# Kernel tuning notes

Measured on AMD Instinct MI355X. Metric: run time of the kernel, lower is better.

The kernel has to match this reference:

```python
import jax, jax.numpy as jnp
import numpy as np
from jax import lax

UNITS = 128
NUM_STEPS = 2048
BATCH = 32
MIN_OMEGA = 0.1
MAX_OMEGA = 70.1
DT = 1.0 / 173.61          # EEG sampling interval
INPUT_SCALER = 0.1
BETA = 0.01
TWO_PI = 2 * 3.1415        # module uses 3.1415, not math.pi


def setup_inputs() -> dict:
    key = jax.random.key(0)
    k1, k2 = jax.random.split(key)
    X_r = jax.random.normal(k1, (BATCH, NUM_STEPS, UNITS), dtype=jnp.float32)
    X_i = jax.random.normal(k2, (BATCH, NUM_STEPS, UNITS), dtype=jnp.float32)
    omegas = (jnp.linspace(MIN_OMEGA, MAX_OMEGA, UNITS) * TWO_PI).astype(jnp.float32)[None, :]  # [1, U]
    return {"X_r": X_r, "X_i": X_i, "omegas": omegas}


def reference(X_r, X_i, omegas):
    B, T, U = X_r.shape
    r0 = jnp.ones((B, U), dtype=X_r.dtype)
    phi0 = jnp.zeros((B, U), dtype=X_r.dtype)

    def step(carry, xs):
        r, phi = carry
        xr, xi = xs  # [B, U] each
        input_r = INPUT_SCALER * xr * jnp.cos(phi)
        input_phi = INPUT_SCALER * xi * jnp.sin(phi)
        r = r + ((1.0 - BETA * jnp.square(r)) * r + input_r) * DT
        phi = phi + (omegas - input_phi) * DT
        return (r, phi), (r, phi)

    xs = (jnp.transpose(X_r, (1, 0, 2)), jnp.transpose(X_i, (1, 0, 2)))  # [T, B, U]
    _, (r_seq, phi_seq) = lax.scan(step, (r0, phi0), xs)
    r = jnp.transpose(r_seq, (1, 0, 2))    # [B, T, U]
    phi = jnp.transpose(phi_seq, (1, 0, 2))
    z_real = r * jnp.cos(phi)
    z_imag = r * jnp.sin(phi)
    return (z_real, z_imag)
```

## Files before the change

### kernel.cpp

```cpp
#include <hip/hip_runtime.h>
#include <math.h>

namespace {
constexpr int kUnits = 128;
constexpr int kSteps = 2048;
constexpr int kBatch = 32;
constexpr int kSeg = 16;
constexpr int kNSeg = kSteps / kSeg;
constexpr int kUBlk = 16;
constexpr int kUPT = 2;
constexpr int kUG = kUBlk / kUPT;
constexpr int kThreads = kUG * kNSeg;
constexpr int kBlocks = kBatch * (kUnits / kUBlk);
constexpr int kGrp = 16;
constexpr int kGrpSeg = kNSeg / kGrp;
constexpr int kPad = kUBlk + 1;
constexpr double kDT = 1.0 / 173.61;
constexpr double kTwoPi = 6.283185307179586;
constexpr double kInv2Pi = 1.0 / kTwoPi;
constexpr size_t kChainElems = (size_t)kSteps * kUnits;

typedef float v2f __attribute__((ext_vector_type(2)));

struct Tables {
  float G[kSteps];
  float Gseg[kNSeg];
  float Gg[kGrp];
  float rbar0[kNSeg];
};
constexpr Tables make_tables() {
  Tables tb{};
  double r = 1.0;
  for (int t = 0; t < kSteps; ++t) {
    if (t % kSeg == 0) tb.rbar0[t / kSeg] = (float)r;
    tb.G[t] = (float)(1.0 + (1.0 - 0.03 * r * r) * kDT);
    r = r + (1.0 - 0.01 * r * r) * r * kDT;
  }
  for (int s = 0; s < kNSeg; ++s) {
    double p = 1.0;
    for (int j = 0; j < kSeg; ++j) p *= (double)tb.G[s * kSeg + j];
    tb.Gseg[s] = (float)p;
  }
  for (int g = 0; g < kGrp; ++g) {
    double p = 1.0;
    for (int s = 0; s < kGrpSeg; ++s) p *= (double)tb.Gseg[g * kGrpSeg + s];
    tb.Gg[g] = (float)p;
  }
  return tb;
}
}

__constant__ Tables kTab = make_tables();

__global__ __launch_bounds__(kThreads)
void hopf_fused(const float* __restrict__ Xr, const float* __restrict__ Xi,
                const float* __restrict__ Om,
                float* __restrict__ Zr, float* __restrict__ Zi) {
  __shared__ float sG[kNSeg][kPad];
  __shared__ float sH[kNSeg][kPad];
  __shared__ float sP[kNSeg][kPad];
  __shared__ float sQ[kNSeg][kPad];
  __shared__ float cG[kGrp][kPad], cH[kGrp][kPad], cP[kGrp][kPad], cQ[kGrp][kPad];
  __shared__ float pD[kGrp][kPad], pR[kGrp][kPad];

  const int tid = threadIdx.x;
  const int ug = tid & (kUG - 1);
  const int seg = tid >> 3;
  const int b = blockIdx.x >> 3;
  const int uq = blockIdx.x & 7;
  const int u0 = uq * kUBlk + ug * kUPT;
  const int t0 = seg * kSeg;

  float cw[kUPT], sw[kUPT], c0[kUPT], s0[kUPT];
  double wdt_d[kUPT];
#pragma unroll
  for (int k = 0; k < kUPT; ++k) {
    const double wdt = (double)Om[u0 + k] * kDT;
    wdt_d[k] = wdt;
    double sd, cd;
    sincos(wdt, &sd, &cd);
    cw[k] = (float)cd;
    sw[k] = (float)sd;
    const double ang = wdt * (double)t0;
    const double kk = rint(ang * kInv2Pi);
    const float th = (float)fma(-kk, kTwoPi, ang);
    __sincosf(th, &s0[k], &c0[k]);
  }

  const size_t base = ((size_t)b * kSteps + t0) * (size_t)kUnits + u0;
  const v2f* xr2 = (const v2f*)(Xr + base);
  const v2f* xi2 = (const v2f*)(Xi + base);
  v2f xr[kSeg], xi[kSeg];
#pragma unroll
  for (int j = 0; j < kSeg; ++j) {
    xr[j] = xr2[j * (kUnits / 2)];
    xi[j] = xi2[j * (kUnits / 2)];
  }

  const float cdt = (float)(0.1 * kDT);
  float gr[kUPT] = {1.f, 1.f}, hr[kUPT] = {0.f, 0.f};
  float pr[kUPT] = {0.f, 0.f}, qr[kUPT] = {0.f, 0.f};
#pragma unroll
  for (int j = 0; j < kSeg; ++j) {
    const float Ge = kTab.G[t0 + j];
#pragma unroll
    for (int k = 0; k < kUPT; ++k) {
      const float axi = cdt * xi[j][k];
      const float axr = cdt * xr[j][k];
      const float ge = fmaf(-axi, c0[k], 1.f);
      const float he = -axi * s0[k];
      const float pe = -axr * s0[k];
      const float qe = axr * c0[k];
      const float g2 = gr[k] * ge;
      const float h2 = fmaf(ge, hr[k], he);
      const float p2 = fmaf(pe, gr[k], Ge * pr[k]);
      const float q2 = fmaf(pe, hr[k], fmaf(Ge, qr[k], qe));
      gr[k] = g2; hr[k] = h2; pr[k] = p2; qr[k] = q2;
      const float c1 = fmaf(cw[k], c0[k], -(sw[k] * s0[k]));
      const float s1 = fmaf(cw[k], s0[k], sw[k] * c0[k]);
      c0[k] = c1; s0[k] = s1;
    }
  }
#pragma unroll
  for (int k = 0; k < kUPT; ++k) {
    const int ch = ug * kUPT + k;
    sG[seg][ch] = gr[k];
    sH[seg][ch] = hr[k];
    sP[seg][ch] = pr[k];
    sQ[seg][ch] = qr[k];
  }
  __syncthreads();

  if (tid < kUBlk * kGrp) {
    const int ch = tid & (kUBlk - 1);
    const int gb = tid >> 4;
    float g = 1.f, h = 0.f, p = 0.f, q = 0.f;
#pragma unroll
    for (int i = 0; i < kGrpSeg; ++i) {
      const int sg = gb * kGrpSeg + i;
      const float mg = sG[sg][ch], mh = sH[sg][ch];
      const float mp = sP[sg][ch], mq = sQ[sg][ch];
      const float Gs = kTab.Gseg[sg];
      const float g2 = mg * g;
      const float h2 = fmaf(mg, h, mh);
      const float p2 = fmaf(mp, g, Gs * p);
      const float q2 = fmaf(mp, h, fmaf(Gs, q, mq));
      g = g2; h = h2; p = p2; q = q2;
    }
    cG[gb][ch] = g; cH[gb][ch] = h; cP[gb][ch] = p; cQ[gb][ch] = q;
  }
  __syncthreads();

  if (tid < kUBlk) {
    const int ch = tid;
    float d = 0.f, rho = 0.f;
#pragma unroll
    for (int gb = 0; gb < kGrp; ++gb) {
      pD[gb][ch] = d;
      pR[gb][ch] = rho;
      const float g = cG[gb][ch], h = cH[gb][ch];
      const float p = cP[gb][ch], q = cQ[gb][ch];
      const float Gs = kTab.Gg[gb];
      const float dn = fmaf(g, d, h);
      const float rn = fmaf(p, d, fmaf(Gs, rho, q));
      d = dn; rho = rn;
    }
  }
  __syncthreads();

  if (tid < kUBlk * kGrp) {
    const int ch = tid & (kUBlk - 1);
    const int gb = tid >> 4;
    float d = pD[gb][ch], rho = pR[gb][ch];
#pragma unroll
    for (int i = 0; i < kGrpSeg; ++i) {
      const int sg = gb * kGrpSeg + i;
      const float mg = sG[sg][ch], mh = sH[sg][ch];
      const float mp = sP[sg][ch], mq = sQ[sg][ch];
      sG[sg][ch] = d;
      sH[sg][ch] = rho;
      const float Gs = kTab.Gseg[sg];
      const float dn = fmaf(mg, d, mh);
      const float rn = fmaf(mp, d, fmaf(Gs, rho, mq));
      d = dn; rho = rn;
    }
  }
  __syncthreads();

  float c[kUPT], s[kUPT], r[kUPT];
#pragma unroll
  for (int k = 0; k < kUPT; ++k) {
    const int ch = ug * kUPT + k;
    const float delta = sG[seg][ch];
    const float rho = sH[seg][ch];
    const double ang = wdt_d[k] * (double)t0 + (double)delta;
    const double kk = rint(ang * kInv2Pi);
    const float th = (float)fma(-kk, kTwoPi, ang);
    __sincosf(th, &s[k], &c[k]);
    r[k] = kTab.rbar0[seg] + rho;
  }

  const float DTf = (float)kDT;
  const float nscale = -(0.1f * DTf);
  const float c01dt = 0.1f * DTf;
  v2f* zr2 = (v2f*)(Zr + base);
  v2f* zi2 = (v2f*)(Zi + base);
#pragma unroll
  for (int j = 0; j < kSeg; ++j) {
    v2f ozr, ozi;
#pragma unroll
    for (int k = 0; k < kUPT; ++k) {
      const float eps = (xi[j][k] * nscale) * s[k];
      const float A = fmaf(-sw[k], eps, cw[k]);
      const float B = fmaf(cw[k], eps, sw[k]);
      const float c2 = fmaf(A, c[k], -(B * s[k]));
      const float s2 = fmaf(A, s[k], B * c[k]);
      const float rr = r[k] * r[k];
      const float om1 = fmaf(-0.01f, rr, 1.f);
      const float racc = fmaf(xr[j][k] * c[k], c01dt, r[k]);
      r[k] = fmaf(om1 * r[k], DTf, racc);
      c[k] = c2; s[k] = s2;
      ozr[k] = r[k] * c[k];
      ozi[k] = r[k] * s[k];
    }
    __builtin_nontemporal_store(ozr, &zr2[j * (kUnits / 2)]);
    __builtin_nontemporal_store(ozi, &zi2[j * (kUnits / 2)]);
  }
}

extern "C" void kernel_launch(void* const* d_in, const int* in_sizes, int n_in,
                              void* d_out, int out_size, void* d_ws, size_t ws_size,
                              hipStream_t stream) {
  const float* Xr = (const float*)d_in[0];
  const float* Xi = (const float*)d_in[1];
  const float* Om = (const float*)d_in[2];
  float* Zr = (float*)d_out;
  float* Zi = (float*)d_out + (size_t)kBatch * kChainElems;

  hipLaunchKernelGGL(hopf_fused, dim3(kBlocks), dim3(kThreads), 0, stream,
                     Xr, Xi, Om, Zr, Zi);
}
```

Baseline: 129.8 us.

## Use one unit per thread with longer segments and remapped block order

Each thread now handles a single unit over 32 steps instead of two units over 16 steps, and each block covers 8 units instead of 16. The block index is remapped so neighbouring blocks cover adjacent unit halves, and the per-unit rotation sincos is computed once in shared memory. A minimum of 4 blocks per CU is requested via launch bounds. The aim is to change work distribution and occupancy, at the cost of scalar 4-byte loads and stores in place of 8-byte vectors and a longer serial chain per thread.

```diff
diff --git a/kernel.cpp b/kernel.cpp
--- a/kernel.cpp
+++ b/kernel.cpp
@@ -5,10 +5,10 @@
 constexpr int kUnits = 128;
 constexpr int kSteps = 2048;
 constexpr int kBatch = 32;
-constexpr int kSeg = 16;
+constexpr int kSeg = 32;
 constexpr int kNSeg = kSteps / kSeg;
-constexpr int kUBlk = 16;
-constexpr int kUPT = 2;
+constexpr int kUBlk = 8;
+constexpr int kUPT = 1;
 constexpr int kUG = kUBlk / kUPT;
 constexpr int kThreads = kUG * kNSeg;
 constexpr int kBlocks = kBatch * (kUnits / kUBlk);
@@ -19,8 +19,6 @@
 constexpr double kTwoPi = 6.283185307179586;
 constexpr double kInv2Pi = 1.0 / kTwoPi;
 constexpr size_t kChainElems = (size_t)kSteps * kUnits;
-
-typedef float v2f __attribute__((ext_vector_type(2)));
 
 struct Tables {
   float G[kSteps];
@@ -52,7 +50,7 @@
 
 __constant__ Tables kTab = make_tables();
 
-__global__ __launch_bounds__(kThreads)
+__global__ __launch_bounds__(kThreads, 4)
 void hopf_fused(const float* __restrict__ Xr, const float* __restrict__ Xi,
                 const float* __restrict__ Om,
                 float* __restrict__ Zr, float* __restrict__ Zi) {
@@ -62,78 +60,75 @@
   __shared__ float sQ[kNSeg][kPad];
   __shared__ float cG[kGrp][kPad], cH[kGrp][kPad], cP[kGrp][kPad], cQ[kGrp][kPad];
   __shared__ float pD[kGrp][kPad], pR[kGrp][kPad];
+  __shared__ float cwS[kUBlk], swS[kUBlk];
 
   const int tid = threadIdx.x;
   const int ug = tid & (kUG - 1);
   const int seg = tid >> 3;
-  const int b = blockIdx.x >> 3;
-  const int uq = blockIdx.x & 7;
-  const int u0 = uq * kUBlk + ug * kUPT;
+  const int xg = blockIdx.x & 7;
+  const int half = (blockIdx.x >> 3) & 1;
+  const int b = (blockIdx.x >> 4) & 31;
+  const int uq = xg * 2 + half;
+  const int u0 = uq * kUBlk + ug;
   const int t0 = seg * kSeg;
 
-  float cw[kUPT], sw[kUPT], c0[kUPT], s0[kUPT];
-  double wdt_d[kUPT];
-#pragma unroll
-  for (int k = 0; k < kUPT; ++k) {
-    const double wdt = (double)Om[u0 + k] * kDT;
-    wdt_d[k] = wdt;
+  if (tid < kUBlk) {
+    const double wdt = (double)Om[uq * kUBlk + tid] * kDT;
     double sd, cd;
     sincos(wdt, &sd, &cd);
-    cw[k] = (float)cd;
-    sw[k] = (float)sd;
-    const double ang = wdt * (double)t0;
+    cwS[tid] = (float)cd;
+    swS[tid] = (float)sd;
+  }
+
+  const double wdt_d = (double)Om[u0] * kDT;
+  float c0, s0;
+  {
+    const double ang = wdt_d * (double)t0;
     const double kk = rint(ang * kInv2Pi);
     const float th = (float)fma(-kk, kTwoPi, ang);
-    __sincosf(th, &s0[k], &c0[k]);
-  }
+    __sincosf(th, &s0, &c0);
+  }
+  __syncthreads();
+  const float cw = cwS[ug];
+  const float sw = swS[ug];
 
   const size_t base = ((size_t)b * kSteps + t0) * (size_t)kUnits + u0;
-  const v2f* xr2 = (const v2f*)(Xr + base);
-  const v2f* xi2 = (const v2f*)(Xi + base);
-  v2f xr[kSeg], xi[kSeg];
+  float xr[kSeg], xi[kSeg];
 #pragma unroll
   for (int j = 0; j < kSeg; ++j) {
-    xr[j] = xr2[j * (kUnits / 2)];
-    xi[j] = xi2[j * (kUnits / 2)];
+    xr[j] = Xr[base + (size_t)j * kUnits];
+    xi[j] = Xi[base + (size_t)j * kUnits];
   }
 
   const float cdt = (float)(0.1 * kDT);
-  float gr[kUPT] = {1.f, 1.f}, hr[kUPT] = {0.f, 0.f};
-  float pr[kUPT] = {0.f, 0.f}, qr[kUPT] = {0.f, 0.f};
+  float gr = 1.f, hr = 0.f, pr = 0.f, qr = 0.f;
 #pragma unroll
   for (int j = 0; j < kSeg; ++j) {
     const float Ge = kTab.G[t0 + j];
-#pragma unroll
-    for (int k = 0; k < kUPT; ++k) {
-      const float axi = cdt * xi[j][k];
-      const float axr = cdt * xr[j][k];
-      const float ge = fmaf(-axi, c0[k], 1.f);
-      const float he = -axi * s0[k];
-      const float pe = -axr * s0[k];
-      const float qe = axr * c0[k];
-      const float g2 = gr[k] * ge;
-      const float h2 = fmaf(ge, hr[k], he);
-      const float p2 = fmaf(pe, gr[k], Ge * pr[k]);
-      const float q2 = fmaf(pe, hr[k], fmaf(Ge, qr[k], qe));
-      gr[k] = g2; hr[k] = h2; pr[k] = p2; qr[k] = q2;
-      const float c1 = fmaf(cw[k], c0[k], -(sw[k] * s0[k]));
-      const float s1 = fmaf(cw[k], s0[k], sw[k] * c0[k]);
-      c0[k] = c1; s0[k] = s1;
-    }
-  }
-#pragma unroll
-  for (int k = 0; k < kUPT; ++k) {
-    const int ch = ug * kUPT + k;
-    sG[seg][ch] = gr[k];
-    sH[seg][ch] = hr[k];
-    sP[seg][ch] = pr[k];
-    sQ[seg][ch] = qr[k];
-  }
+    const float axi = cdt * xi[j];
+    const float axr = cdt * xr[j];
+    const float ge = fmaf(-axi, c0, 1.f);
+    const float he = -axi * s0;
+    const float pe = -axr * s0;
+    const float qe = axr * c0;
+    const float g2 = gr * ge;
+    const float h2 = fmaf(ge, hr, he);
+    const float p2 = fmaf(pe, gr, Ge * pr);
+    const float q2 = fmaf(pe, hr, fmaf(Ge, qr, qe));
+    gr = g2; hr = h2; pr = p2; qr = q2;
+    const float c1 = fmaf(cw, c0, -(sw * s0));
+    const float s1 = fmaf(cw, s0, sw * c0);
+    c0 = c1; s0 = s1;
+  }
+  sG[seg][ug] = gr;
+  sH[seg][ug] = hr;
+  sP[seg][ug] = pr;
+  sQ[seg][ug] = qr;
   __syncthreads();
 
   if (tid < kUBlk * kGrp) {
     const int ch = tid & (kUBlk - 1);
-    const int gb = tid >> 4;
+    const int gb = tid >> 3;
     float g = 1.f, h = 0.f, p = 0.f, q = 0.f;
 #pragma unroll
     for (int i = 0; i < kGrpSeg; ++i) {
@@ -170,7 +165,7 @@
 
   if (tid < kUBlk * kGrp) {
     const int ch = tid & (kUBlk - 1);
-    const int gb = tid >> 4;
+    const int gb = tid >> 3;
     float d = pD[gb][ch], rho = pR[gb][ch];
 #pragma unroll
     for (int i = 0; i < kGrpSeg; ++i) {
@@ -187,44 +182,34 @@
   }
   __syncthreads();
 
-  float c[kUPT], s[kUPT], r[kUPT];
-#pragma unroll
-  for (int k = 0; k < kUPT; ++k) {
-    const int ch = ug * kUPT + k;
-    const float delta = sG[seg][ch];
-    const float rho = sH[seg][ch];
-    const double ang = wdt_d[k] * (double)t0 + (double)delta;
+  float c, s, r;
+  {
+    const float delta = sG[seg][ug];
+    const float rho = sH[seg][ug];
+    const double ang = wdt_d * (double)t0 + (double)delta;
     const double kk = rint(ang * kInv2Pi);
     const float th = (float)fma(-kk, kTwoPi, ang);
-    __sincosf(th, &s[k], &c[k]);
-    r[k] = kTab.rbar0[seg] + rho;
+    __sincosf(th, &s, &c);
+    r = kTab.rbar0[seg] + rho;
   }
 
   const float DTf = (float)kDT;
   const float nscale = -(0.1f * DTf);
   const float c01dt = 0.1f * DTf;
-  v2f* zr2 = (v2f*)(Zr + base);
-  v2f* zi2 = (v2f*)(Zi + base);
 #pragma unroll
   for (int j = 0; j < kSeg; ++j) {
-    v2f ozr, ozi;
-#pragma unroll
-    for (int k = 0; k < kUPT; ++k) {
-      const float eps = (xi[j][k] * nscale) * s[k];
-      const float A = fmaf(-sw[k], eps, cw[k]);
-      const float B = fmaf(cw[k], eps, sw[k]);
-      const float c2 = fmaf(A, c[k], -(B * s[k]));
-      const float s2 = fmaf(A, s[k], B * c[k]);
-      const float rr = r[k] * r[k];
-      const float om1 = fmaf(-0.01f, rr, 1.f);
-      const float racc = fmaf(xr[j][k] * c[k], c01dt, r[k]);
-      r[k] = fmaf(om1 * r[k], DTf, racc);
-      c[k] = c2; s[k] = s2;
-      ozr[k] = r[k] * c[k];
-      ozi[k] = r[k] * s[k];
-    }
-    __builtin_nontemporal_store(ozr, &zr2[j * (kUnits / 2)]);
-    __builtin_nontemporal_store(ozi, &zi2[j * (kUnits / 2)]);
+    const float eps = (xi[j] * nscale) * s;
+    const float A = fmaf(-sw, eps, cw);
+    const float B = fmaf(cw, eps, sw);
+    const float c2 = fmaf(A, c, -(B * s));
+    const float s2 = fmaf(A, s, B * c);
+    const float rr = r * r;
+    const float om1 = fmaf(-0.01f, rr, 1.f);
+    const float racc = fmaf(xr[j] * c, c01dt, r);
+    r = fmaf(om1 * r, DTf, racc);
+    c = c2; s = s2;
+    __builtin_nontemporal_store(r * c, Zr + base + (size_t)j * kUnits);
+    __builtin_nontemporal_store(r * s, Zi + base + (size_t)j * kUnits);
   }
 }
 
```

New measurement: 164.6 us. 26.9% more time.
